# Kernel optimization log

Measured on AMD Instinct MI355X. Metric: run time of the kernel, lower is better.

## Reference

```python
import jax, jax.numpy as jnp
import numpy as np

EMBED_DIM = 1024
NUM_HEADS = 16
HEAD_DIM = EMBED_DIM // NUM_HEADS
NUM_GLOBAL = 2
NUM_RANDOM = 3
WINDOW_SIZE = 3
B, S = 2, 2048


def setup_inputs() -> dict:
    key = jax.random.key(0)
    ks = jax.random.split(key, 10)
    scale = 0.02
    inp = {
        "x": jax.random.normal(ks[0], (B, S, EMBED_DIM), dtype=jnp.float32),
        "random_indices": jax.random.randint(ks[1], (S, NUM_RANDOM), 0, S, dtype=jnp.int32),
        "q_w": jax.random.normal(ks[2], (EMBED_DIM, EMBED_DIM), dtype=jnp.float32) * scale,
        "q_b": jnp.zeros((EMBED_DIM,), dtype=jnp.float32),
        "k_w": jax.random.normal(ks[3], (EMBED_DIM, EMBED_DIM), dtype=jnp.float32) * scale,
        "k_b": jnp.zeros((EMBED_DIM,), dtype=jnp.float32),
        "v_w": jax.random.normal(ks[4], (EMBED_DIM, EMBED_DIM), dtype=jnp.float32) * scale,
        "v_b": jnp.zeros((EMBED_DIM,), dtype=jnp.float32),
        "o_w": jax.random.normal(ks[5], (EMBED_DIM, EMBED_DIM), dtype=jnp.float32) * scale,
        "o_b": jnp.zeros((EMBED_DIM,), dtype=jnp.float32),
    }
    return inp


def _build_mask(random_indices, seq_len):
    # [S, S] boolean BigBird mask: global rows/cols + sliding window + random.
    i = jnp.arange(seq_len)[:, None]
    j = jnp.arange(seq_len)[None, :]
    glob = (i < NUM_GLOBAL) | (j < NUM_GLOBAL)
    win = jnp.abs(i - j) <= WINDOW_SIZE
    rand = jnp.zeros((seq_len, seq_len), dtype=bool)
    rows = jnp.repeat(jnp.arange(seq_len), NUM_RANDOM)
    rand = rand.at[rows, random_indices.reshape(-1)].set(True)
    return glob | win | rand


def reference(x, random_indices, q_w, q_b, k_w, k_b, v_w, v_b, o_w, o_b):
    b, s, _ = x.shape
    # torch nn.Linear: y = x @ W.T + b
    q = (x @ q_w.T + q_b).reshape(b, s, NUM_HEADS, HEAD_DIM).transpose(0, 2, 1, 3)
    k = (x @ k_w.T + k_b).reshape(b, s, NUM_HEADS, HEAD_DIM).transpose(0, 2, 1, 3)
    v = (x @ v_w.T + v_b).reshape(b, s, NUM_HEADS, HEAD_DIM).transpose(0, 2, 1, 3)
    scores = jnp.einsum("bhqd,bhkd->bhqk", q, k) / jnp.sqrt(jnp.float32(HEAD_DIM))
    mask = _build_mask(random_indices, s)  # [S, S]
    scores = jnp.where(mask[None, None, :, :], scores, -jnp.inf)
    probs = jax.nn.softmax(scores, axis=-1)
    out = jnp.einsum("bhqk,bhkd->bhqd", probs, v)
    out = out.transpose(0, 2, 1, 3).reshape(b, s, EMBED_DIM)
    return out @ o_w.T + o_b
```

## Files before the change

### kernel.cpp

```cpp
#include <hip/hip_runtime.h>

#define B_  2
#define S_  2048
#define E_  1024
#define H_  16
#define D_  64
#define NGLOB 2
#define NRAND 3
#define WIN 3

typedef __bf16 bf16x8 __attribute__((ext_vector_type(8)));
typedef float  f32x4  __attribute__((ext_vector_type(4)));

__device__ __forceinline__ unsigned short f2bf(float f) {
    unsigned u = __builtin_bit_cast(unsigned, f);
    unsigned r = u + 0x7FFFu + ((u >> 16) & 1u);
    return (unsigned short)(r >> 16);
}
__device__ __forceinline__ float bf2f(unsigned short u) {
    return __builtin_bit_cast(float, (unsigned)u << 16);
}

__device__ __forceinline__ void g2l16(const unsigned short* g, unsigned short* l) {
    __builtin_amdgcn_global_load_lds(
        (const __attribute__((address_space(1))) unsigned*)g,
        (__attribute__((address_space(3))) unsigned*)l, 16, 0, 0);
}

__global__ __launch_bounds__(256)
void convert_all(const float* __restrict__ x,  const float* __restrict__ qw,
                 const float* __restrict__ kw, const float* __restrict__ vw,
                 const float* __restrict__ ow,
                 unsigned short* __restrict__ xb, unsigned short* __restrict__ wqkv,
                 unsigned short* __restrict__ wo) {
    const int XN = (B_ * S_ * E_) / 4;
    const int WN = (E_ * E_) / 4;
    int i = blockIdx.x * blockDim.x + threadIdx.x;
    int r, loc;
    if (i < XN) { r = 0; loc = i; }
    else        { int j = i - XN; r = 1 + (j >> 18); loc = j & (WN - 1); }
    const float* src = r == 0 ? x : r == 1 ? qw : r == 2 ? kw : r == 3 ? vw : ow;
    float4 f = ((const float4*)src)[loc];
    ushort4 u;
    u.x = f2bf(f.x); u.y = f2bf(f.y); u.z = f2bf(f.z); u.w = f2bf(f.w);
    ushort4* dst = r == 0 ? (ushort4*)xb : r == 4 ? (ushort4*)wo
                 : (ushort4*)wqkv + (size_t)(r - 1) * WN;
    dst[loc] = u;
}

__global__ __launch_bounds__(256, 3)
void gemm_qkv(const unsigned short* __restrict__ A,
              const unsigned short* __restrict__ W,
              const float* __restrict__ b0, const float* __restrict__ b1,
              const float* __restrict__ b2,
              unsigned short* __restrict__ Cb, int M, int N, int K) {
    __shared__ unsigned short sA[128 * 64];
    __shared__ unsigned short sB[128 * 64];
    const int nwg = gridDim.x;
    const int id  = (blockIdx.x & 7) * (nwg >> 3) + (blockIdx.x >> 3);
    const int bm = (id & 31) * 128;
    const int bn = (id >> 5) * 128;
    const int t = threadIdx.x;
    const int lane = t & 63;
    const int wave = t >> 6;
    const int wm = wave >> 1, wn = wave & 1;
    const int lq = lane >> 4;
    const int lr = lane & 15;

    f32x4 acc[4][4] = {};

    for (int k0 = 0; k0 < K; k0 += 64) {
        const unsigned short* Abase = A + (size_t)bm * K + k0;
        const unsigned short* Wbase = W + (size_t)bn * K + k0;
        #pragma unroll
        for (int j = 0; j < 4; ++j) {
            int c = j * 256 + t;
            int row = c >> 3, cc = c & 7;
            int gcol = ((cc ^ (row & 7)) << 3);
            int dst = j * 2048 + wave * 512;
            g2l16(Abase + (size_t)row * K + gcol, sA + dst);
            g2l16(Wbase + (size_t)row * K + gcol, sB + dst);
        }
        __syncthreads();

        #pragma unroll
        for (int ks = 0; ks < 2; ++ks) {
            const int sw = (((ks << 2) + lq) ^ (lr & 7)) << 3;
            bf16x8 af[4], bfr[4];
            #pragma unroll
            for (int i = 0; i < 4; ++i)
                af[i] = *(const bf16x8*)&sA[(wm * 64 + i * 16 + lr) * 64 + sw];
            #pragma unroll
            for (int j = 0; j < 4; ++j)
                bfr[j] = *(const bf16x8*)&sB[(wn * 64 + j * 16 + lr) * 64 + sw];
            #pragma unroll
            for (int i = 0; i < 4; ++i)
                #pragma unroll
                for (int j = 0; j < 4; ++j)
                    acc[i][j] = __builtin_amdgcn_mfma_f32_16x16x32_bf16(af[i], bfr[j], acc[i][j], 0, 0, 0);
        }
        __syncthreads();
    }

    #pragma unroll
    for (int i = 0; i < 4; ++i) {
        int row0 = bm + wm * 64 + i * 16 + lq * 4;
        #pragma unroll
        for (int j = 0; j < 4; ++j) {
            int col = bn + wn * 64 + j * 16 + lr;
            const float* bp = col < E_ ? b0 : (col < 2 * E_ ? b1 : b2);
            float bv = bp[col & (E_ - 1)];
            #pragma unroll
            for (int r = 0; r < 4; ++r)
                Cb[(size_t)(row0 + r) * N + col] = f2bf(acc[i][j][r] + bv);
        }
    }
}

__global__ __launch_bounds__(256, 3)
void gemm_o(const unsigned short* __restrict__ A,
            const unsigned short* __restrict__ W,
            const float* __restrict__ bias,
            float* __restrict__ Cf, int M, int N, int K) {
    __shared__ unsigned short sA[128 * 64];
    __shared__ unsigned short sB[128 * 64];
    const int nwg = gridDim.x;
    const int id  = (blockIdx.x & 7) * (nwg >> 3) + (blockIdx.x >> 3);
    const int bm = (id & 31) * 128;
    const int bn = (id >> 5) * 128;
    const int t = threadIdx.x;
    const int lane = t & 63;
    const int wave = t >> 6;
    const int wm = wave >> 1, wn = wave & 1;
    const int lq = lane >> 4;
    const int lr = lane & 15;

    f32x4 acc[4][4] = {};

    for (int k0 = 0; k0 < K; k0 += 64) {
        const unsigned short* Abase = A + (size_t)bm * K + k0;
        const unsigned short* Wbase = W + (size_t)bn * K + k0;
        #pragma unroll
        for (int j = 0; j < 4; ++j) {
            int c = j * 256 + t;
            int row = c >> 3, cc = c & 7;
            int gcol = ((cc ^ (row & 7)) << 3);
            int dst = j * 2048 + wave * 512;
            g2l16(Abase + (size_t)row * K + gcol, sA + dst);
            g2l16(Wbase + (size_t)row * K + gcol, sB + dst);
        }
        __syncthreads();

        #pragma unroll
        for (int ks = 0; ks < 2; ++ks) {
            const int sw = (((ks << 2) + lq) ^ (lr & 7)) << 3;
            bf16x8 af[4], bfr[4];
            #pragma unroll
            for (int i = 0; i < 4; ++i)
                af[i] = *(const bf16x8*)&sA[(wm * 64 + i * 16 + lr) * 64 + sw];
            #pragma unroll
            for (int j = 0; j < 4; ++j)
                bfr[j] = *(const bf16x8*)&sB[(wn * 64 + j * 16 + lr) * 64 + sw];
            #pragma unroll
            for (int i = 0; i < 4; ++i)
                #pragma unroll
                for (int j = 0; j < 4; ++j)
                    acc[i][j] = __builtin_amdgcn_mfma_f32_16x16x32_bf16(af[i], bfr[j], acc[i][j], 0, 0, 0);
        }
        __syncthreads();
    }

    #pragma unroll
    for (int i = 0; i < 4; ++i) {
        int row0 = bm + wm * 64 + i * 16 + lq * 4;
        #pragma unroll
        for (int j = 0; j < 4; ++j) {
            int col = bn + wn * 64 + j * 16 + lr;
            float bv = bias[col];
            #pragma unroll
            for (int r = 0; r < 4; ++r)
                Cf[(size_t)(row0 + r) * N + col] = acc[i][j][r] + bv;
        }
    }
}

__global__ __launch_bounds__(256, 5)
void attn_fused(const unsigned short* __restrict__ qkv,
                const int* __restrict__ rnd,
                float* __restrict__ gaccp, float* __restrict__ gms,
                unsigned short* __restrict__ attn) {
    const int NB = B_ * (S_ - 2);
    int t = threadIdx.x;

    if (blockIdx.x < 256) {
        int g = blockIdx.x;
        int b = g >> 7, ck = g & 127;
        int w = t >> 6, l = t & 63;
        int h = l >> 2, dseg = l & 3;
        int key0 = ck * 16 + w * 4;

        __shared__ float sm[4][16][4];
        __shared__ float ovv[4][2][16][68];

        const unsigned short* qb0 = qkv + (size_t)(b * S_) * 3072 + h * 64 + dseg * 16;
        const unsigned short* qb1 = qb0 + 3072;
        bf16x8 q0a = *(const bf16x8*)qb0, q0b = *(const bf16x8*)(qb0 + 8);
        bf16x8 q1a = *(const bf16x8*)qb1, q1b = *(const bf16x8*)(qb1 + 8);

        const unsigned short* kr0 =
            qkv + (size_t)(b * S_ + key0) * 3072 + E_ + h * 64 + dseg * 16;
        bf16x8 ka[4], kb[4];
        #pragma unroll
        for (int j = 0; j < 4; ++j) {
            ka[j] = *(const bf16x8*)(kr0 + (size_t)j * 3072);
            kb[j] = *(const bf16x8*)(kr0 + (size_t)j * 3072 + 8);
        }
        bf16x8 va0 = *(const bf16x8*)(kr0 + E_);
        bf16x8 vb0 = *(const bf16x8*)(kr0 + E_ + 8);
        bf16x8 va1 = *(const bf16x8*)(kr0 + 3072 + E_);
        bf16x8 vb1 = *(const bf16x8*)(kr0 + 3072 + E_ + 8);

        float s0[4], s1[4];
        #pragma unroll
        for (int j = 0; j < 4; ++j) {
            float a0 = 0.f, a1 = 0.f;
            #pragma unroll
            for (int e = 0; e < 8; ++e) {
                float k1 = (float)ka[j][e], k2 = (float)kb[j][e];
                a0 += (float)q0a[e] * k1 + (float)q0b[e] * k2;
                a1 += (float)q1a[e] * k1 + (float)q1b[e] * k2;
            }
            a0 += __shfl_xor(a0, 1); a0 += __shfl_xor(a0, 2);
            a1 += __shfl_xor(a1, 1); a1 += __shfl_xor(a1, 2);
            s0[j] = a0 * 0.125f; s1[j] = a1 * 0.125f;
        }

        float m0 = fmaxf(fmaxf(s0[0], s0[1]), fmaxf(s0[2], s0[3]));
        float m1 = fmaxf(fmaxf(s1[0], s1[1]), fmaxf(s1[2], s1[3]));
        float e0[4], e1[4], sum0 = 0.f, sum1 = 0.f;
        #pragma unroll
        for (int j = 0; j < 4; ++j) {
            e0[j] = __expf(s0[j] - m0); sum0 += e0[j];
            e1[j] = __expf(s1[j] - m1); sum1 += e1[j];
        }

        bf16x8 va2 = *(const bf16x8*)(kr0 + 2 * 3072 + E_);
        bf16x8 vb2 = *(const bf16x8*)(kr0 + 2 * 3072 + E_ + 8);
        bf16x8 va3 = *(const bf16x8*)(kr0 + 3 * 3072 + E_);
        bf16x8 vb3 = *(const bf16x8*)(kr0 + 3 * 3072 + E_ + 8);

        float o0[16] = {}, o1[16] = {};
        #pragma unroll
        for (int e = 0; e < 8; ++e) {
            float v1 = (float)va0[e], v2 = (float)vb0[e];
            float v3 = (float)va1[e], v4 = (float)vb1[e];
            o0[e]     += e0[0] * v1 + e0[1] * v3;
            o0[8 + e] += e0[0] * v2 + e0[1] * v4;
            o1[e]     += e1[0] * v1 + e1[1] * v3;
            o1[8 + e] += e1[0] * v2 + e1[1] * v4;
        }
        #pragma unroll
        for (int e = 0; e < 8; ++e) {
            float v1 = (float)va2[e], v2 = (float)vb2[e];
            float v3 = (float)va3[e], v4 = (float)vb3[e];
            o0[e]     += e0[2] * v1 + e0[3] * v3;
            o0[8 + e] += e0[2] * v2 + e0[3] * v4;
            o1[e]     += e1[2] * v1 + e1[3] * v3;
            o1[8 + e] += e1[2] * v2 + e1[3] * v4;
        }

        if (dseg == 0) {
            sm[w][h][0] = m0; sm[w][h][1] = sum0;
            sm[w][h][2] = m1; sm[w][h][3] = sum1;
        }
        #pragma unroll
        for (int e = 0; e < 16; ++e) {
            ovv[w][0][h][dseg * 16 + e] = o0[e];
            ovv[w][1][h][dseg * 16 + e] = o1[e];
        }
        __syncthreads();

        #pragma unroll
        for (int r = 0; r < 8; ++r) {
            int ot = r * 256 + t;
            int ii = ot >> 10, hh = (ot >> 6) & 15, d = ot & 63;
            float M = -1e30f;
            #pragma unroll
            for (int ww = 0; ww < 4; ++ww) M = fmaxf(M, sm[ww][hh][ii * 2]);
            float den = 0.f, num = 0.f;
            #pragma unroll
            for (int ww = 0; ww < 4; ++ww) {
                float f = __expf(sm[ww][hh][ii * 2] - M);
                den += sm[ww][hh][ii * 2 + 1] * f;
                num += ovv[ww][ii][hh][d] * f;
            }
            int tup = b * 32 + ii * 16 + hh;
            gaccp[((size_t)tup * 128 + ck) * D_ + d] = num;
            if (d == 0) {
                gms[((size_t)tup * 128 + ck) * 2]     = M;
                gms[((size_t)tup * 128 + ck) * 2 + 1] = den;
            }
        }
        return;
    }

    int bb = blockIdx.x - 256;
    int bidx = (bb & 7) * 128 + (bb >> 3);
    int w = t >> 6, l = t & 63;
    int row = bidx * 4 + w;
    bool valid = row < NB;
    int b = row / (S_ - 2);
    int i = row % (S_ - 2) + 2;
    if (!valid) { b = 0; i = 2; }

    __shared__ int   cols_s[4][12];
    __shared__ int   ncol_sh[4];
    __shared__ float pr_s[4][16 * 13 + 3];

    const bf16x8* qp = (const bf16x8*)(qkv + (size_t)(b * S_ + i) * 3072);
    bf16x8 q0 = qp[l * 2], q1 = qp[l * 2 + 1];
    float qreg[16];
    #pragma unroll
    for (int j = 0; j < 8; ++j) { qreg[j] = (float)q0[j]; qreg[8 + j] = (float)q1[j]; }

    if (l == 0) {
        int* cols = cols_s[w];
        int n = 0;
        cols[n++] = 0; cols[n++] = 1;
        int lo = i - WIN; if (lo < NGLOB) lo = NGLOB;
        int hi = i + WIN; if (hi > S_ - 1) hi = S_ - 1;
        for (int j = lo; j <= hi; ++j) cols[n++] = j;
        for (int r = 0; r < NRAND; ++r) {
            int c = rnd[i * NRAND + r];
            bool dup = false;
            for (int q = 0; q < n; ++q) dup = dup || (cols[q] == c);
            if (!dup) cols[n++] = c;
        }
        ncol_sh[w] = n;
        for (int q = n; q < 12; ++q) cols[q] = 0;
    }
    __syncthreads();
    const int n = ncol_sh[w];
    const int h4 = l >> 2;

    float sco[12];
    #pragma unroll
    for (int c = 0; c < 12; ++c) {
        const bf16x8* kp = (const bf16x8*)(qkv + (size_t)(b * S_ + cols_s[w][c]) * 3072 + E_);
        bf16x8 k0 = kp[l * 2], k1 = kp[l * 2 + 1];
        float s = 0.f;
        #pragma unroll
        for (int j = 0; j < 8; ++j) s += qreg[j] * (float)k0[j] + qreg[8 + j] * (float)k1[j];
        s += __shfl_xor(s, 1);
        s += __shfl_xor(s, 2);
        sco[c] = (c < n) ? s * 0.125f : -1e30f;
    }

    if ((l & 3) == 0) {
        float m = -1e30f;
        #pragma unroll
        for (int c = 0; c < 12; ++c) m = fmaxf(m, sco[c]);
        float sum = 0.f;
        #pragma unroll
        for (int c = 0; c < 12; ++c) { float e = __expf(sco[c] - m); sco[c] = e; sum += e; }
        float inv = 1.f / sum;
        #pragma unroll
        for (int c = 0; c < 12; ++c) pr_s[w][h4 * 13 + c] = sco[c] * inv;
    }
    __syncthreads();

    float o[16] = {};
    #pragma unroll
    for (int c = 0; c < 12; ++c) {
        float p = pr_s[w][h4 * 13 + c];
        const bf16x8* vp = (const bf16x8*)(qkv + (size_t)(b * S_ + cols_s[w][c]) * 3072 + 2 * E_);
        bf16x8 v0 = vp[l * 2], v1 = vp[l * 2 + 1];
        #pragma unroll
        for (int j = 0; j < 8; ++j) { o[j] += p * (float)v0[j]; o[8 + j] += p * (float)v1[j]; }
    }

    if (valid) {
        ushort4 u0, u1, u2, u3;
        u0.x = f2bf(o[0]);  u0.y = f2bf(o[1]);  u0.z = f2bf(o[2]);  u0.w = f2bf(o[3]);
        u1.x = f2bf(o[4]);  u1.y = f2bf(o[5]);  u1.z = f2bf(o[6]);  u1.w = f2bf(o[7]);
        u2.x = f2bf(o[8]);  u2.y = f2bf(o[9]);  u2.z = f2bf(o[10]); u2.w = f2bf(o[11]);
        u3.x = f2bf(o[12]); u3.y = f2bf(o[13]); u3.z = f2bf(o[14]); u3.w = f2bf(o[15]);
        ushort4* op = (ushort4*)(attn + (size_t)(b * S_ + i) * E_ + l * 16);
        op[0] = u0; op[1] = u1; op[2] = u2; op[3] = u3;
    }
}

__global__ __launch_bounds__(256)
void gattn_fin(const float* __restrict__ gaccp, const float* __restrict__ gms,
               unsigned short* __restrict__ attn) {
    int tup = blockIdx.x;
    int b = tup >> 5, i = (tup >> 4) & 1, h = tup & 15;
    int t = threadIdx.x, g = t >> 6, d = t & 63;
    __shared__ float sM[4], sD[4], sO[4][D_];

    float M = -1e30f;
    #pragma unroll 8
    for (int c = g * 32; c < g * 32 + 32; ++c)
        M = fmaxf(M, gms[((size_t)tup * 128 + c) * 2]);
    float den = 0.f, num = 0.f;
    #pragma unroll 8
    for (int c = g * 32; c < g * 32 + 32; ++c) {
        float f = __expf(gms[((size_t)tup * 128 + c) * 2] - M);
        den += gms[((size_t)tup * 128 + c) * 2 + 1] * f;
        num += gaccp[((size_t)tup * 128 + c) * D_ + d] * f;
    }
    if (d == 0) { sM[g] = M; sD[g] = den; }
    sO[g][d] = num;
    __syncthreads();
    if (g == 0) {
        float MM = fmaxf(fmaxf(sM[0], sM[1]), fmaxf(sM[2], sM[3]));
        float dd = 0.f, nn = 0.f;
        #pragma unroll
        for (int j = 0; j < 4; ++j) {
            float f = __expf(sM[j] - MM);
            dd += sD[j] * f;
            nn += sO[j][d] * f;
        }
        attn[(size_t)(b * S_ + i) * E_ + h * D_ + d] = f2bf(nn / dd);
    }
}

extern "C" void kernel_launch(void* const* d_in, const int* in_sizes, int n_in,
                              void* d_out, int out_size, void* d_ws, size_t ws_size,
                              hipStream_t stream) {
    const float* x   = (const float*)d_in[0];
    const int*   rnd = (const int*)d_in[1];
    const float* qw  = (const float*)d_in[2];
    const float* qb  = (const float*)d_in[3];
    const float* kw  = (const float*)d_in[4];
    const float* kb  = (const float*)d_in[5];
    const float* vw  = (const float*)d_in[6];
    const float* vb  = (const float*)d_in[7];
    const float* ow  = (const float*)d_in[8];
    const float* ob  = (const float*)d_in[9];
    float* out = (float*)d_out;

    char* ws = (char*)d_ws;
    unsigned short* xb    = (unsigned short*)(ws);
    unsigned short* wqkv  = (unsigned short*)(ws + 8388608);
    unsigned short* wo    = (unsigned short*)(ws + 14680064);
    unsigned short* qkv   = (unsigned short*)(ws + 16777216);
    unsigned short* attn  = (unsigned short*)(ws + 41943040);
    float*          gaccp = (float*)(ws);
    float*          gms   = (float*)(ws + 2097152);

    const int M = B_ * S_;

    {
        int total4 = (M * E_ + 4 * E_ * E_) / 4;
        convert_all<<<total4 / 256, 256, 0, stream>>>(x, qw, kw, vw, ow, xb, wqkv, wo);
    }

    gemm_qkv<<<768, 256, 0, stream>>>(xb, wqkv, qb, kb, vb, qkv, M, 3 * E_, E_);

    attn_fused<<<256 + 1024, 256, 0, stream>>>(qkv, rnd, gaccp, gms, attn);

    gattn_fin<<<64, 256, 0, stream>>>(gaccp, gms, attn);

    gemm_o<<<256, 256, 0, stream>>>(attn, wo, ob, out, M, E_, E_);
}
```

Baseline: 169.6 us.

## Rewrite QKV GEMM with 256x256 tiles and double-buffered async LDS pipeline

The QKV projection GEMM moves from 128x128 tiles with 256 threads and a single LDS buffer to 256x256 tiles with 512 threads (8 waves). The new kernel double-buffers the A and W tiles in LDS, staging the next K-slices with global_load_lds while MFMAs run, split into four interleaved phases using explicit waitcnt, sched_barrier and setprio. The goal is to hide global-load latency and raise arithmetic intensity per block. In exchange it uses 128KB of LDS per block and launches only 192 blocks, which can leave some CUs idle.

```diff
diff --git a/kernel.cpp b/kernel.cpp
--- a/kernel.cpp
+++ b/kernel.cpp
@@ -48,71 +48,162 @@
     dst[loc] = u;
 }
 
-__global__ __launch_bounds__(256, 3)
+__device__ __forceinline__ void stage_half(const unsigned short* g, unsigned short* l,
+                                           int t, int wave, int K) {
+    #pragma unroll
+    for (int j = 0; j < 2; ++j) {
+        int c = j * 512 + t;
+        int row = c >> 3, cc = c & 7;
+        g2l16(g + (size_t)row * K + ((cc ^ (row & 7)) << 3), l + j * 4096 + wave * 512);
+    }
+}
+__device__ __forceinline__ bf16x8 ldfrag(const unsigned short* r, int row, int kc) {
+    return *(const bf16x8*)&r[row * 64 + ((kc ^ (row & 7)) << 3)];
+}
+
+__global__ __launch_bounds__(512, 2)
 void gemm_qkv(const unsigned short* __restrict__ A,
               const unsigned short* __restrict__ W,
-              const float* __restrict__ b0, const float* __restrict__ b1,
-              const float* __restrict__ b2,
+              const float* __restrict__ bi0, const float* __restrict__ bi1,
+              const float* __restrict__ bi2,
               unsigned short* __restrict__ Cb, int M, int N, int K) {
-    __shared__ unsigned short sA[128 * 64];
-    __shared__ unsigned short sB[128 * 64];
-    const int nwg = gridDim.x;
-    const int id  = (blockIdx.x & 7) * (nwg >> 3) + (blockIdx.x >> 3);
-    const int bm = (id & 31) * 128;
-    const int bn = (id >> 5) * 128;
+    __shared__ unsigned short lds[2][4][128 * 64];
     const int t = threadIdx.x;
     const int lane = t & 63;
     const int wave = t >> 6;
-    const int wm = wave >> 1, wn = wave & 1;
+    const int wr = wave >> 2;
+    const int wc = wave & 3;
     const int lq = lane >> 4;
     const int lr = lane & 15;
-
-    f32x4 acc[4][4] = {};
-
-    for (int k0 = 0; k0 < K; k0 += 64) {
-        const unsigned short* Abase = A + (size_t)bm * K + k0;
-        const unsigned short* Wbase = W + (size_t)bn * K + k0;
-        #pragma unroll
-        for (int j = 0; j < 4; ++j) {
-            int c = j * 256 + t;
-            int row = c >> 3, cc = c & 7;
-            int gcol = ((cc ^ (row & 7)) << 3);
-            int dst = j * 2048 + wave * 512;
-            g2l16(Abase + (size_t)row * K + gcol, sA + dst);
-            g2l16(Wbase + (size_t)row * K + gcol, sB + dst);
-        }
-        __syncthreads();
-
-        #pragma unroll
-        for (int ks = 0; ks < 2; ++ks) {
-            const int sw = (((ks << 2) + lq) ^ (lr & 7)) << 3;
-            bf16x8 af[4], bfr[4];
-            #pragma unroll
-            for (int i = 0; i < 4; ++i)
-                af[i] = *(const bf16x8*)&sA[(wm * 64 + i * 16 + lr) * 64 + sw];
-            #pragma unroll
-            for (int j = 0; j < 4; ++j)
-                bfr[j] = *(const bf16x8*)&sB[(wn * 64 + j * 16 + lr) * 64 + sw];
-            #pragma unroll
-            for (int i = 0; i < 4; ++i)
+    const int bm = blockIdx.x * 256;
+    const int bn = blockIdx.y * 256;
+    const int nt = K >> 6;
+
+    const unsigned short* Ab = A + (size_t)bm * K;
+    const unsigned short* Wb = W + (size_t)bn * K;
+
+    f32x4 acc[8][4] = {};
+
+    stage_half(Ab,                         &lds[0][0][0], t, wave, K);
+    stage_half(Ab + (size_t)128 * K,       &lds[0][1][0], t, wave, K);
+    stage_half(Wb,                         &lds[0][2][0], t, wave, K);
+    stage_half(Wb + (size_t)128 * K,       &lds[0][3][0], t, wave, K);
+    stage_half(Wb + 64,                    &lds[1][2][0], t, wave, K);
+    stage_half(Wb + (size_t)128 * K + 64,  &lds[1][3][0], t, wave, K);
+    asm volatile("s_waitcnt vmcnt(4)" ::: "memory");
+    __builtin_amdgcn_s_barrier();
+
+    #pragma unroll 2
+    for (int kt = 0; kt < nt; ++kt) {
+        const int cur = kt & 1;
+        const unsigned short* rA = &lds[cur][wr][0];
+        const unsigned short* rB = &lds[cur][2 + (wc >> 1)][0];
+        const int brow = (wc & 1) * 64;
+        bf16x8 af[2][2], bfr[4][2];
+
+        #pragma unroll
+        for (int m = 0; m < 2; ++m)
+            #pragma unroll
+            for (int ks = 0; ks < 2; ++ks)
+                af[m][ks] = ldfrag(rA, m * 16 + lr, ks * 4 + lq);
+        #pragma unroll
+        for (int n = 0; n < 4; ++n)
+            #pragma unroll
+            for (int ks = 0; ks < 2; ++ks)
+                bfr[n][ks] = ldfrag(rB, brow + n * 16 + lr, ks * 4 + lq);
+        if (kt + 1 < nt)
+            stage_half(Ab + (size_t)(kt + 1) * 64, &lds[cur ^ 1][0][0], t, wave, K);
+        __builtin_amdgcn_s_barrier();
+        asm volatile("s_waitcnt lgkmcnt(0)" ::: "memory");
+        __builtin_amdgcn_sched_barrier(0);
+        __builtin_amdgcn_s_setprio(1);
+        #pragma unroll
+        for (int m = 0; m < 2; ++m)
+            #pragma unroll
+            for (int n = 0; n < 4; ++n)
                 #pragma unroll
-                for (int j = 0; j < 4; ++j)
-                    acc[i][j] = __builtin_amdgcn_mfma_f32_16x16x32_bf16(af[i], bfr[j], acc[i][j], 0, 0, 0);
-        }
-        __syncthreads();
+                for (int ks = 0; ks < 2; ++ks)
+                    acc[m][n] = __builtin_amdgcn_mfma_f32_16x16x32_bf16(af[m][ks], bfr[n][ks], acc[m][n], 0, 0, 0);
+        __builtin_amdgcn_s_setprio(0);
+        __builtin_amdgcn_s_barrier();
+
+        #pragma unroll
+        for (int m = 0; m < 2; ++m)
+            #pragma unroll
+            for (int ks = 0; ks < 2; ++ks)
+                af[m][ks] = ldfrag(rA, (2 + m) * 16 + lr, ks * 4 + lq);
+        if (kt + 1 < nt)
+            stage_half(Ab + (size_t)128 * K + (size_t)(kt + 1) * 64, &lds[cur ^ 1][1][0], t, wave, K);
+        if (kt + 2 < nt)
+            stage_half(Wb + (size_t)(kt + 2) * 64, &lds[cur][2][0], t, wave, K);
+        __builtin_amdgcn_s_barrier();
+        asm volatile("s_waitcnt lgkmcnt(0)" ::: "memory");
+        __builtin_amdgcn_sched_barrier(0);
+        __builtin_amdgcn_s_setprio(1);
+        #pragma unroll
+        for (int m = 0; m < 2; ++m)
+            #pragma unroll
+            for (int n = 0; n < 4; ++n)
+                #pragma unroll
+                for (int ks = 0; ks < 2; ++ks)
+                    acc[2 + m][n] = __builtin_amdgcn_mfma_f32_16x16x32_bf16(af[m][ks], bfr[n][ks], acc[2 + m][n], 0, 0, 0);
+        __builtin_amdgcn_s_setprio(0);
+        __builtin_amdgcn_s_barrier();
+
+        #pragma unroll
+        for (int m = 0; m < 2; ++m)
+            #pragma unroll
+            for (int ks = 0; ks < 2; ++ks)
+                af[m][ks] = ldfrag(rA, (4 + m) * 16 + lr, ks * 4 + lq);
+        if (kt + 2 < nt)
+            stage_half(Wb + (size_t)128 * K + (size_t)(kt + 2) * 64, &lds[cur][3][0], t, wave, K);
+        __builtin_amdgcn_s_barrier();
+        asm volatile("s_waitcnt lgkmcnt(0)" ::: "memory");
+        __builtin_amdgcn_sched_barrier(0);
+        __builtin_amdgcn_s_setprio(1);
+        #pragma unroll
+        for (int m = 0; m < 2; ++m)
+            #pragma unroll
+            for (int n = 0; n < 4; ++n)
+                #pragma unroll
+                for (int ks = 0; ks < 2; ++ks)
+                    acc[4 + m][n] = __builtin_amdgcn_mfma_f32_16x16x32_bf16(af[m][ks], bfr[n][ks], acc[4 + m][n], 0, 0, 0);
+        __builtin_amdgcn_s_setprio(0);
+        __builtin_amdgcn_s_barrier();
+
+        #pragma unroll
+        for (int m = 0; m < 2; ++m)
+            #pragma unroll
+            for (int ks = 0; ks < 2; ++ks)
+                af[m][ks] = ldfrag(rA, (6 + m) * 16 + lr, ks * 4 + lq);
+        __builtin_amdgcn_s_barrier();
+        asm volatile("s_waitcnt lgkmcnt(0)" ::: "memory");
+        __builtin_amdgcn_sched_barrier(0);
+        __builtin_amdgcn_s_setprio(1);
+        #pragma unroll
+        for (int m = 0; m < 2; ++m)
+            #pragma unroll
+            for (int n = 0; n < 4; ++n)
+                #pragma unroll
+                for (int ks = 0; ks < 2; ++ks)
+                    acc[6 + m][n] = __builtin_amdgcn_mfma_f32_16x16x32_bf16(af[m][ks], bfr[n][ks], acc[6 + m][n], 0, 0, 0);
+        __builtin_amdgcn_s_setprio(0);
+        if (kt + 2 < nt) asm volatile("s_waitcnt vmcnt(4)" ::: "memory");
+        else             asm volatile("s_waitcnt vmcnt(0)" ::: "memory");
+        __builtin_amdgcn_s_barrier();
     }
 
     #pragma unroll
-    for (int i = 0; i < 4; ++i) {
-        int row0 = bm + wm * 64 + i * 16 + lq * 4;
-        #pragma unroll
-        for (int j = 0; j < 4; ++j) {
-            int col = bn + wn * 64 + j * 16 + lr;
-            const float* bp = col < E_ ? b0 : (col < 2 * E_ ? b1 : b2);
+    for (int m = 0; m < 8; ++m) {
+        int row0 = bm + wr * 128 + m * 16 + lq * 4;
+        #pragma unroll
+        for (int n = 0; n < 4; ++n) {
+            int col = bn + wc * 64 + n * 16 + lr;
+            const float* bp = col < E_ ? bi0 : (col < 2 * E_ ? bi1 : bi2);
             float bv = bp[col & (E_ - 1)];
             #pragma unroll
             for (int r = 0; r < 4; ++r)
-                Cb[(size_t)(row0 + r) * N + col] = f2bf(acc[i][j][r] + bv);
+                Cb[(size_t)(row0 + r) * N + col] = f2bf(acc[m][n][r] + bv);
         }
     }
 }
@@ -456,7 +547,10 @@
         convert_all<<<total4 / 256, 256, 0, stream>>>(x, qw, kw, vw, ow, xb, wqkv, wo);
     }
 
-    gemm_qkv<<<768, 256, 0, stream>>>(xb, wqkv, qb, kb, vb, qkv, M, 3 * E_, E_);
+    {
+        dim3 grid(M / 256, 3 * E_ / 256);
+        gemm_qkv<<<grid, 512, 0, stream>>>(xb, wqkv, qb, kb, vb, qkv, M, 3 * E_, E_);
+    }
 
     attn_fused<<<256 + 1024, 256, 0, stream>>>(qkv, rnd, gaccp, gms, attn);
 
```

Measured after the change: 177.6 us. +4.8%, slower.
